# Kernel tuning notes

Hardware: AMD Instinct MI355X
Metric: run time of the kernel (lower is better)

## Reference

```python
import jax, jax.numpy as jnp
import numpy as np

D = 512          # model_dim
H = 4 * D        # hidden_mult * model_dim
E = 8            # n_experts
TEMP = 1.0       # temperature
EPS = 1e-5       # torch LayerNorm eps


def setup_inputs() -> dict:
    key = jax.random.key(0)
    ks = jax.random.split(key, 6)
    x = jax.random.normal(ks[0], (4, 4096, D), dtype=jnp.float32)
    # gate: LayerNorm(D) + Linear(D, E)
    gate_gamma = jnp.ones((D,), jnp.float32)
    gate_beta = jnp.zeros((D,), jnp.float32)
    gate_W = jax.random.normal(ks[1], (D, E), jnp.float32) * 0.02
    gate_b = jnp.zeros((E,), jnp.float32)
    # experts stacked along leading E axis: Linear(D,H) -> LeakyReLU -> Linear(H,D)
    W1 = jax.random.normal(ks[2], (E, D, H), jnp.float32) * 0.02
    b1 = jnp.zeros((E, H), jnp.float32)
    W2 = jax.random.normal(ks[3], (E, H, D), jnp.float32) * 0.02
    b2 = jnp.zeros((E, D), jnp.float32)
    return {"x": x, "gate_gamma": gate_gamma, "gate_beta": gate_beta,
            "gate_W": gate_W, "gate_b": gate_b,
            "W1": W1, "b1": b1, "W2": W2, "b2": b2}


def reference(x, gate_gamma, gate_beta, gate_W, gate_b, W1, b1, W2, b2):
    # gate: LayerNorm then Linear, temperature-scaled softmax
    mu = jnp.mean(x, axis=-1, keepdims=True)
    var = jnp.var(x, axis=-1, keepdims=True)  # biased, as in torch LayerNorm
    xn = (x - mu) * jax.lax.rsqrt(var + EPS) * gate_gamma + gate_beta
    logits = (xn @ gate_W + gate_b) / TEMP          # [B,N,E]
    w = jax.nn.softmax(logits, axis=-1)             # [B,N,E]
    # run every expert on all tokens (faithful to soft routing)
    h = jnp.einsum('bnd,edh->benh', x, W1) + b1[None, :, None, :]  # [B,E,N,H]
    h = jax.nn.leaky_relu(h, negative_slope=0.01)
    y = jnp.einsum('benh,ehd->bend', h, W2) + b2[None, :, None, :]  # [B,E,N,D]
    # gate-weighted combine over experts
    out = jnp.einsum('bend,bne->bnd', y, w)
    return out
```

## Files before the change

### kernel.cpp

```cpp
#include <hip/hip_runtime.h>
#include <stdint.h>

#define TD 512
#define TH 2048
#define TE 8
#define TT 16384

typedef __bf16 bf16x8 __attribute__((ext_vector_type(8)));
typedef __bf16 bf16x4 __attribute__((ext_vector_type(4)));
typedef float  f32x4  __attribute__((ext_vector_type(4)));

__device__ __forceinline__ void async16(const void* src, void* lds) {
    __builtin_amdgcn_global_load_lds((const __attribute__((address_space(1))) uint32_t*)src,
                                     (__attribute__((address_space(3))) uint32_t*)lds,
                                     16, 0, 0);
}

__global__ __launch_bounds__(256) void gate_kernel(
    const float* __restrict__ x, const float* __restrict__ gamma,
    const float* __restrict__ beta, const float* __restrict__ gW,
    const float* __restrict__ gb, const float* __restrict__ b2,
    float* __restrict__ gate_w, __bf16* __restrict__ xb,
    float* __restrict__ outp)
{
    const int t    = blockIdx.x * 4 + (threadIdx.x >> 6);
    const int lane = threadIdx.x & 63;

    const float* xr = x + (size_t)t * TD + lane * 8;
    float4 v0 = *(const float4*)xr;
    float4 v1 = *(const float4*)(xr + 4);
    float xv[8] = {v0.x, v0.y, v0.z, v0.w, v1.x, v1.y, v1.z, v1.w};

    float s = 0.f, sq = 0.f;
    #pragma unroll
    for (int j = 0; j < 8; ++j) { s += xv[j]; sq += xv[j] * xv[j]; }
    #pragma unroll
    for (int off = 32; off > 0; off >>= 1) {
        s  += __shfl_xor(s, off);
        sq += __shfl_xor(sq, off);
    }
    const float mean = s * (1.f / TD);
    const float var  = sq * (1.f / TD) - mean * mean;
    const float rs   = rsqrtf(var + 1e-5f);

    bf16x8 xc;
    #pragma unroll
    for (int j = 0; j < 8; ++j) xc[j] = (__bf16)xv[j];
    *(bf16x8*)&xb[(size_t)t * TD + lane * 8] = xc;

    float p[TE] = {};
    #pragma unroll
    for (int j = 0; j < 8; ++j) {
        const int d = lane * 8 + j;
        const float xn = (xv[j] - mean) * rs * gamma[d] + beta[d];
        const float* wr = gW + (size_t)d * TE;
        #pragma unroll
        for (int e = 0; e < TE; ++e) p[e] += xn * wr[e];
    }
    #pragma unroll
    for (int off = 32; off > 0; off >>= 1) {
        #pragma unroll
        for (int e = 0; e < TE; ++e) p[e] += __shfl_xor(p[e], off);
    }

    float m = -3.4e38f;
    #pragma unroll
    for (int e = 0; e < TE; ++e) { p[e] += gb[e]; m = fmaxf(m, p[e]); }
    float sum = 0.f;
    #pragma unroll
    for (int e = 0; e < TE; ++e) { p[e] = expf(p[e] - m); sum += p[e]; }
    const float inv = 1.f / sum;
    if (lane == 0) {
        #pragma unroll
        for (int e = 0; e < TE; ++e) gate_w[(size_t)t * TE + e] = p[e] * inv;
    }

    float ob[8] = {};
    #pragma unroll
    for (int e = 0; e < TE; ++e) {
        const float we = p[e] * inv;
        const float* b2r = b2 + (size_t)e * TD + lane * 8;
        #pragma unroll
        for (int j = 0; j < 8; ++j) ob[j] += we * b2r[j];
    }
    float4 o0 = {ob[0], ob[1], ob[2], ob[3]};
    float4 o1 = {ob[4], ob[5], ob[6], ob[7]};
    *(float4*)&outp[(size_t)t * TD + lane * 8]     = o0;
    *(float4*)&outp[(size_t)t * TD + lane * 8 + 4] = o1;
}

template <int MODE>
__global__ __launch_bounds__(256) void tcast(
    const float* __restrict__ src, __bf16* __restrict__ dst, int R, int C)
{
    __shared__ __bf16 tile[64][65];
    const int e  = blockIdx.z;
    const int r0 = blockIdx.y * 64, c0 = blockIdx.x * 64;
    const int tr = threadIdx.x >> 6;
    const int tc = threadIdx.x & 63;

    const float* s = src + ((size_t)e * R + r0) * C + c0;
    #pragma unroll
    for (int i = 0; i < 16; ++i) {
        const int r = i * 4 + tr;
        tile[r][tc] = (__bf16)s[(size_t)r * C + tc];
    }
    __syncthreads();

    size_t RS, eoff;
    if (MODE == 0) { RS = (size_t)R;     eoff = (size_t)e * C * R; }
    else           { RS = (size_t)2 * R; eoff = (size_t)(e >> 1) * C * 2 * R + (size_t)(e & 1) * R; }

    __bf16* d = dst + eoff + (size_t)c0 * RS + r0;
    #pragma unroll
    for (int i = 0; i < 16; ++i) {
        const int c = i * 4 + tr;
        d[(size_t)c * RS + tc] = tile[tc][c];
    }
}

template <int EPI>
__global__ __launch_bounds__(256, 2) void gemm2b(
    const __bf16* __restrict__ A, const __bf16* __restrict__ Bt,
    const float* __restrict__ b1, const float* __restrict__ gw,
    void* __restrict__ C, int grp)
{
    constexpr int S  = (EPI == 0) ? TD : 2 * TH;
    constexpr int NT = (EPI == 0) ? 16 : 64;

    __shared__ __align__(16) char smem[49152];

    const int tid  = threadIdx.x;
    const int w    = tid >> 6, lane = tid & 63;
    const int fr   = lane & 15, ks = lane >> 4;

    int bm, bn, e2 = 0, e = 0;
    if (EPI == 0) {
        const int xcd = blockIdx.x & 7, idx = blockIdx.x >> 3;
        bm = xcd * 16 + (idx & 15);
        const int pn = idx >> 4;
        e2 = pn >> 3;
        bn = pn & 7;
        e  = grp * 2 + e2;
        A  += (size_t)bm * 128 * S;
        Bt += (size_t)e2 * TH * TD + (size_t)bn * 256 * S;
        b1 += (size_t)e * TH;
    } else {
        const int xcd = blockIdx.x & 7, idx = blockIdx.x >> 3;
        bm = xcd * 16 + (idx & 15);
        const int pn = idx >> 4;
        const int kh = pn >> 1;
        bn = pn & 1;
        A  += (size_t)bm * 128 * S + (size_t)kh * 2048;
        Bt += (size_t)bn * 256 * S + (size_t)kh * 2048;
    }

    const __bf16* Ab = A;
    const __bf16* Bb = Bt;

    f32x4 acc[8][4] = {};

    auto stage = [&](int t, int b) {
        char* aRegion = smem + b * 8192;
        char* bRegion = smem + 16384 + b * 16384;
        #pragma unroll
        for (int p = 0; p < 2; ++p) {
            const int cid = p * 256 + tid;
            const int row = cid >> 2;
            const int gc  = (cid & 3) ^ ((row >> 1) & 3);
            async16(Ab + (size_t)row * S + t * 32 + gc * 8, aRegion + cid * 16);
        }
        #pragma unroll
        for (int p = 0; p < 4; ++p) {
            const int cid = p * 256 + tid;
            const int row = cid >> 2;
            const int gc  = (cid & 3) ^ ((row >> 1) & 3);
            async16(Bb + (size_t)row * S + t * 32 + gc * 8, bRegion + cid * 16);
        }
    };

    stage(0, 0);
    stage(1, 1);

    for (int t = 0; t < NT; ++t) {
        const int buf = t & 1;
        const char* aR = smem + buf * 8192;
        const char* bR = smem + 16384 + buf * 16384;

        if (t + 1 < NT) { asm volatile("s_waitcnt vmcnt(6)" ::: "memory"); }
        else            { asm volatile("s_waitcnt vmcnt(0)" ::: "memory"); }
        __builtin_amdgcn_sched_barrier(0);
        __builtin_amdgcn_s_barrier();

        bf16x8 areg[8], breg[4];
        #pragma unroll
        for (int m = 0; m < 8; ++m) {
            const int row = m * 16 + fr;
            areg[m] = *(const bf16x8*)(aR + row * 64 + (((ks ^ (row >> 1)) & 3) << 4));
        }
        #pragma unroll
        for (int n = 0; n < 4; ++n) {
            const int row = w * 64 + n * 16 + fr;
            breg[n] = *(const bf16x8*)(bR + row * 64 + (((ks ^ (row >> 1)) & 3) << 4));
        }
        asm volatile("s_waitcnt lgkmcnt(0)" ::: "memory");
        __builtin_amdgcn_sched_barrier(0);
        __builtin_amdgcn_s_barrier();

        if (t + 2 < NT) stage(t + 2, buf);

        __builtin_amdgcn_s_setprio(1);
        #pragma unroll
        for (int m = 0; m < 8; ++m)
            #pragma unroll
            for (int n = 0; n < 4; ++n) {
                if (EPI == 0)
                    acc[m][n] = __builtin_amdgcn_mfma_f32_16x16x32_bf16(breg[n], areg[m], acc[m][n], 0, 0, 0);
                else
                    acc[m][n] = __builtin_amdgcn_mfma_f32_16x16x32_bf16(areg[m], breg[n], acc[m][n], 0, 0, 0);
            }
        __builtin_amdgcn_s_setprio(0);
        __builtin_amdgcn_sched_barrier(0);
    }

    if (EPI == 0) {
        __bf16* hC = (__bf16*)C;
        const int rjc = (lane >> 4) << 2;
        #pragma unroll
        for (int m = 0; m < 8; ++m) {
            const int row = bm * 128 + m * 16 + fr;
            const float wgt = gw[(size_t)row * TE + e];
            __bf16* hrow = hC + (size_t)row * (2 * TH) + e2 * TH;
            #pragma unroll
            for (int n = 0; n < 4; ++n) {
                const int colb = bn * 256 + w * 64 + n * 16 + rjc;
                const f32x4 bv = *(const f32x4*)&b1[colb];
                bf16x4 ov;
                #pragma unroll
                for (int j = 0; j < 4; ++j) {
                    float v = acc[m][n][j] + bv[j];
                    v = v > 0.f ? v : 0.01f * v;
                    ov[j] = (__bf16)(v * wgt);
                }
                *(bf16x4*)&hrow[colb] = ov;
            }
        }
    } else {
        float* oC = (float*)C;
        const int rj = (lane >> 4) << 2;
        #pragma unroll
        for (int m = 0; m < 8; ++m) {
            const int gr0 = bm * 128 + m * 16 + rj;
            #pragma unroll
            for (int j = 0; j < 4; ++j) {
                const int gr = gr0 + j;
                #pragma unroll
                for (int n = 0; n < 4; ++n) {
                    const int gc = bn * 256 + w * 64 + n * 16 + fr;
                    atomicAdd(oC + (size_t)gr * TD + gc, acc[m][n][j]);
                }
            }
        }
    }
}

extern "C" void kernel_launch(void* const* d_in, const int* in_sizes, int n_in,
                              void* d_out, int out_size, void* d_ws, size_t ws_size,
                              hipStream_t stream)
{
    const float* x     = (const float*)d_in[0];
    const float* gamma = (const float*)d_in[1];
    const float* beta  = (const float*)d_in[2];
    const float* gW    = (const float*)d_in[3];
    const float* gb    = (const float*)d_in[4];
    const float* W1    = (const float*)d_in[5];
    const float* b1    = (const float*)d_in[6];
    const float* W2    = (const float*)d_in[7];
    const float* b2    = (const float*)d_in[8];

    char* ws = (char*)d_ws;
    size_t off = 0;
    float*  gate_w = (float*)(ws + off);  off += (size_t)TT * TE * 4;
    __bf16* xb     = (__bf16*)(ws + off); off += (size_t)TT * TD * 2;
    __bf16* W1t    = (__bf16*)(ws + off); off += (size_t)TE * TD * TH * 2;
    __bf16* W2tc   = (__bf16*)(ws + off); off += (size_t)TE * TD * TH * 2;
    __bf16* h      = (__bf16*)(ws + off);

    gate_kernel<<<TT / 4, 256, 0, stream>>>(x, gamma, beta, gW, gb, b2,
                                            gate_w, xb, (float*)d_out);
    tcast<0><<<dim3(TH / 64, TD / 64, TE), 256, 0, stream>>>(W1, W1t, TD, TH);
    tcast<1><<<dim3(TD / 64, TH / 64, TE), 256, 0, stream>>>(W2, W2tc, TH, TD);

    for (int grp = 0; grp < 4; ++grp) {
        gemm2b<0><<<2048, 256, 0, stream>>>(
            xb, W1t + (size_t)grp * 2 * TH * TD, b1, gate_w, (void*)h, grp);
        gemm2b<1><<<512, 256, 0, stream>>>(
            h, W2tc + (size_t)grp * TD * 2 * TH, nullptr, nullptr, d_out, grp);
    }
}
```

Baseline: 847.4 us.

## Load B fragments straight to registers and shrink GEMM tile to 128x128

```diff
diff --git a/kernel.cpp b/kernel.cpp
--- a/kernel.cpp
+++ b/kernel.cpp
@@ -120,7 +120,7 @@
 }
 
 template <int EPI>
-__global__ __launch_bounds__(256, 2) void gemm2b(
+__global__ __launch_bounds__(256, 3) void gemm_rb(
     const __bf16* __restrict__ A, const __bf16* __restrict__ Bt,
     const float* __restrict__ b1, const float* __restrict__ gw,
     void* __restrict__ C, int grp)
@@ -128,112 +128,111 @@
     constexpr int S  = (EPI == 0) ? TD : 2 * TH;
     constexpr int NT = (EPI == 0) ? 16 : 64;
 
-    __shared__ __align__(16) char smem[49152];
+    __shared__ __align__(16) char smem[16384];
 
     const int tid  = threadIdx.x;
     const int w    = tid >> 6, lane = tid & 63;
+    const int wr   = w >> 1, wc = w & 1;
     const int fr   = lane & 15, ks = lane >> 4;
 
     int bm, bn, e2 = 0, e = 0;
     if (EPI == 0) {
-        const int xcd = blockIdx.x & 7, idx = blockIdx.x >> 3;
-        bm = xcd * 16 + (idx & 15);
-        const int pn = idx >> 4;
-        e2 = pn >> 3;
-        bn = pn & 7;
+        bm = blockIdx.x & 127;
+        const int r = blockIdx.x >> 7;
+        bn = r & 15;
+        e2 = r >> 4;
         e  = grp * 2 + e2;
         A  += (size_t)bm * 128 * S;
-        Bt += (size_t)e2 * TH * TD + (size_t)bn * 256 * S;
+        Bt += (size_t)e2 * TH * TD;
         b1 += (size_t)e * TH;
     } else {
-        const int xcd = blockIdx.x & 7, idx = blockIdx.x >> 3;
-        bm = xcd * 16 + (idx & 15);
-        const int pn = idx >> 4;
-        const int kh = pn >> 1;
-        bn = pn & 1;
+        bm = blockIdx.x & 127;
+        const int r = blockIdx.x >> 7;
+        bn = r & 3;
+        const int kh = r >> 2;
         A  += (size_t)bm * 128 * S + (size_t)kh * 2048;
-        Bt += (size_t)bn * 256 * S + (size_t)kh * 2048;
+        Bt += (size_t)kh * 2048;
     }
 
     const __bf16* Ab = A;
-    const __bf16* Bb = Bt;
-
-    f32x4 acc[8][4] = {};
-
-    auto stage = [&](int t, int b) {
-        char* aRegion = smem + b * 8192;
-        char* bRegion = smem + 16384 + b * 16384;
+    const __bf16* Bp = Bt + ((size_t)bn * 128 + wc * 64 + fr) * S + ks * 8;
+
+    f32x4 acc[4][4] = {};
+
+    auto stageA = [&](int t, char* region) {
         #pragma unroll
         for (int p = 0; p < 2; ++p) {
             const int cid = p * 256 + tid;
             const int row = cid >> 2;
             const int gc  = (cid & 3) ^ ((row >> 1) & 3);
-            async16(Ab + (size_t)row * S + t * 32 + gc * 8, aRegion + cid * 16);
-        }
-        #pragma unroll
-        for (int p = 0; p < 4; ++p) {
-            const int cid = p * 256 + tid;
-            const int row = cid >> 2;
-            const int gc  = (cid & 3) ^ ((row >> 1) & 3);
-            async16(Bb + (size_t)row * S + t * 32 + gc * 8, bRegion + cid * 16);
+            async16(Ab + (size_t)row * S + t * 32 + gc * 8, region + cid * 16);
         }
     };
-
-    stage(0, 0);
-    stage(1, 1);
-
-    for (int t = 0; t < NT; ++t) {
-        const int buf = t & 1;
-        const char* aR = smem + buf * 8192;
-        const char* bR = smem + 16384 + buf * 16384;
-
-        if (t + 1 < NT) { asm volatile("s_waitcnt vmcnt(6)" ::: "memory"); }
+    auto loadB = [&](int t, bf16x8 (&dst)[4]) {
+        #pragma unroll
+        for (int n = 0; n < 4; ++n)
+            dst[n] = *(const bf16x8*)(Bp + (size_t)n * 16 * S + t * 32);
+    };
+
+    auto iter = [&](int t, char* buf, bf16x8 (&cur)[4], bf16x8 (&nxt)[4]) {
+        if (t + 1 < NT) { asm volatile("s_waitcnt vmcnt(2)" ::: "memory"); }
         else            { asm volatile("s_waitcnt vmcnt(0)" ::: "memory"); }
         __builtin_amdgcn_sched_barrier(0);
         __builtin_amdgcn_s_barrier();
 
-        bf16x8 areg[8], breg[4];
-        #pragma unroll
-        for (int m = 0; m < 8; ++m) {
-            const int row = m * 16 + fr;
-            areg[m] = *(const bf16x8*)(aR + row * 64 + (((ks ^ (row >> 1)) & 3) << 4));
-        }
-        #pragma unroll
-        for (int n = 0; n < 4; ++n) {
-            const int row = w * 64 + n * 16 + fr;
-            breg[n] = *(const bf16x8*)(bR + row * 64 + (((ks ^ (row >> 1)) & 3) << 4));
+        bf16x8 areg[4];
+        #pragma unroll
+        for (int m = 0; m < 4; ++m) {
+            const int row = wr * 64 + m * 16 + fr;
+            areg[m] = *(const bf16x8*)(buf + row * 64 + (((ks ^ (row >> 1)) & 3) << 4));
         }
         asm volatile("s_waitcnt lgkmcnt(0)" ::: "memory");
         __builtin_amdgcn_sched_barrier(0);
         __builtin_amdgcn_s_barrier();
 
-        if (t + 2 < NT) stage(t + 2, buf);
+        if (t + 1 < NT) loadB(t + 1, nxt);
+        __builtin_amdgcn_sched_barrier(0);
+        if (t + 2 < NT) stageA(t + 2, buf);
+        __builtin_amdgcn_sched_barrier(0);
 
         __builtin_amdgcn_s_setprio(1);
         #pragma unroll
-        for (int m = 0; m < 8; ++m)
+        for (int m = 0; m < 4; ++m)
             #pragma unroll
             for (int n = 0; n < 4; ++n) {
                 if (EPI == 0)
-                    acc[m][n] = __builtin_amdgcn_mfma_f32_16x16x32_bf16(breg[n], areg[m], acc[m][n], 0, 0, 0);
+                    acc[m][n] = __builtin_amdgcn_mfma_f32_16x16x32_bf16(cur[n], areg[m], acc[m][n], 0, 0, 0);
                 else
-                    acc[m][n] = __builtin_amdgcn_mfma_f32_16x16x32_bf16(areg[m], breg[n], acc[m][n], 0, 0, 0);
+                    acc[m][n] = __builtin_amdgcn_mfma_f32_16x16x32_bf16(areg[m], cur[n], acc[m][n], 0, 0, 0);
             }
         __builtin_amdgcn_s_setprio(0);
         __builtin_amdgcn_sched_barrier(0);
+    };
+
+    bf16x8 bregA[4], bregB[4];
+    char* buf0 = smem;
+    char* buf1 = smem + 8192;
+
+    loadB(0, bregA);
+    stageA(0, buf0);
+    stageA(1, buf1);
+
+    for (int tt = 0; tt < NT; tt += 2) {
+        iter(tt,     buf0, bregA, bregB);
+        iter(tt + 1, buf1, bregB, bregA);
     }
 
     if (EPI == 0) {
         __bf16* hC = (__bf16*)C;
         const int rjc = (lane >> 4) << 2;
         #pragma unroll
-        for (int m = 0; m < 8; ++m) {
-            const int row = bm * 128 + m * 16 + fr;
+        for (int m = 0; m < 4; ++m) {
+            const int row = bm * 128 + wr * 64 + m * 16 + fr;
             const float wgt = gw[(size_t)row * TE + e];
             __bf16* hrow = hC + (size_t)row * (2 * TH) + e2 * TH;
             #pragma unroll
             for (int n = 0; n < 4; ++n) {
-                const int colb = bn * 256 + w * 64 + n * 16 + rjc;
+                const int colb = bn * 128 + wc * 64 + n * 16 + rjc;
                 const f32x4 bv = *(const f32x4*)&b1[colb];
                 bf16x4 ov;
                 #pragma unroll
@@ -249,14 +248,14 @@
         float* oC = (float*)C;
         const int rj = (lane >> 4) << 2;
         #pragma unroll
-        for (int m = 0; m < 8; ++m) {
-            const int gr0 = bm * 128 + m * 16 + rj;
+        for (int m = 0; m < 4; ++m) {
+            const int gr0 = bm * 128 + wr * 64 + m * 16 + rj;
             #pragma unroll
             for (int j = 0; j < 4; ++j) {
                 const int gr = gr0 + j;
                 #pragma unroll
                 for (int n = 0; n < 4; ++n) {
-                    const int gc = bn * 256 + w * 64 + n * 16 + fr;
+                    const int gc = bn * 128 + wc * 64 + n * 16 + fr;
                     atomicAdd(oC + (size_t)gr * TD + gc, acc[m][n][j]);
                 }
             }
@@ -292,9 +291,9 @@
     tcast<1><<<dim3(TD / 64, TH / 64, TE), 256, 0, stream>>>(W2, W2tc, TH, TD);
 
     for (int grp = 0; grp < 4; ++grp) {
-        gemm2b<0><<<2048, 256, 0, stream>>>(
+        gemm_rb<0><<<4096, 256, 0, stream>>>(
             xb, W1t + (size_t)grp * 2 * TH * TD, b1, gate_w, (void*)h, grp);
-        gemm2b<1><<<512, 256, 0, stream>>>(
+        gemm_rb<1><<<1024, 256, 0, stream>>>(
             h, W2tc + (size_t)grp * TD * 2 * TH, nullptr, nullptr, d_out, grp);
     }
 }
```

Result: slower. 1.432 ms (+69.0%).

## Keep A tile resident in LDS for first GEMM and stream all B panels

Applied to the files above, without the earlier changes.

```diff
diff --git a/kernel.cpp b/kernel.cpp
--- a/kernel.cpp
+++ b/kernel.cpp
@@ -119,14 +119,124 @@
     }
 }
 
-template <int EPI>
-__global__ __launch_bounds__(256, 2) void gemm2b(
+__global__ __launch_bounds__(512, 2) void gemm1res(
     const __bf16* __restrict__ A, const __bf16* __restrict__ Bt,
     const float* __restrict__ b1, const float* __restrict__ gw,
-    void* __restrict__ C, int grp)
-{
-    constexpr int S  = (EPI == 0) ? TD : 2 * TH;
-    constexpr int NT = (EPI == 0) ? 16 : 64;
+    __bf16* __restrict__ hC, int grp)
+{
+    __shared__ __align__(16) char smem[163840];
+    char* Asm = smem;
+    char* Bsm = smem + 131072;
+
+    const int tid  = threadIdx.x;
+    const int w    = tid >> 6, lane = tid & 63;
+    const int wr   = w >> 2, wc = w & 3;
+    const int fr   = lane & 15, ks = lane >> 4;
+
+    const int bm = blockIdx.x & 127;
+    const int e2 = blockIdx.x >> 7;
+    const int e  = grp * 2 + e2;
+
+    const __bf16* Ab  = A  + (size_t)bm * 128 * TD;
+    const __bf16* Bb  = Bt + (size_t)e2 * TH * TD;
+    const float*  b1e = b1 + (size_t)e * TH;
+
+    #pragma unroll
+    for (int q = 0; q < 16; ++q) {
+        const int cid = q * 512 + tid;
+        const int row = cid >> 6;
+        const int c   = cid & 63;
+        async16(Ab + (size_t)row * TD + (size_t)(c ^ (row & 7)) * 8,
+                Asm + cid * 16);
+    }
+
+    auto stageB = [&](int bt, char* region) {
+        const int p = bt >> 4, kt = bt & 15;
+        const __bf16* Bp = Bb + (size_t)p * 256 * TD + kt * 32;
+        #pragma unroll
+        for (int q = 0; q < 2; ++q) {
+            const int cid = q * 512 + tid;
+            const int row = cid >> 2;
+            const int c   = cid & 3;
+            async16(Bp + (size_t)row * TD + (size_t)(c ^ ((row >> 1) & 3)) * 8,
+                    region + cid * 16);
+        }
+    };
+
+    stageB(0, Bsm);
+    stageB(1, Bsm + 16384);
+
+    f32x4 acc[4][4] = {};
+    constexpr int BT = 128;
+
+    for (int bt = 0; bt < BT; ++bt) {
+        const int kt = bt & 15;
+        char* buf = Bsm + (bt & 1) * 16384;
+
+        if (bt + 1 < BT) { asm volatile("s_waitcnt vmcnt(2)" ::: "memory"); }
+        else             { asm volatile("s_waitcnt vmcnt(0)" ::: "memory"); }
+        __builtin_amdgcn_sched_barrier(0);
+        __builtin_amdgcn_s_barrier();
+        __builtin_amdgcn_sched_barrier(0);
+
+        bf16x8 areg[4], breg[4];
+        #pragma unroll
+        for (int m = 0; m < 4; ++m) {
+            const int row = wr * 64 + m * 16 + fr;
+            const int c   = kt * 4 + ks;
+            areg[m] = *(const bf16x8*)(Asm + row * 1024 + (size_t)((c ^ (row & 7)) << 4));
+        }
+        #pragma unroll
+        for (int n = 0; n < 4; ++n) {
+            const int row = wc * 64 + n * 16 + fr;
+            breg[n] = *(const bf16x8*)(buf + row * 64 + (((ks ^ (row >> 1)) & 3) << 4));
+        }
+        __builtin_amdgcn_s_setprio(1);
+        #pragma unroll
+        for (int m = 0; m < 4; ++m)
+            #pragma unroll
+            for (int n = 0; n < 4; ++n)
+                acc[m][n] = __builtin_amdgcn_mfma_f32_16x16x32_bf16(breg[n], areg[m], acc[m][n], 0, 0, 0);
+        __builtin_amdgcn_s_setprio(0);
+        __builtin_amdgcn_sched_barrier(0);
+        __builtin_amdgcn_s_barrier();
+        __builtin_amdgcn_sched_barrier(0);
+
+        if (bt + 2 < BT) stageB(bt + 2, buf);
+
+        if (kt == 15) {
+            const int p   = bt >> 4;
+            const int rjc = (lane >> 4) << 2;
+            #pragma unroll
+            for (int m = 0; m < 4; ++m) {
+                const int row = bm * 128 + wr * 64 + m * 16 + fr;
+                const float wgt = gw[(size_t)row * TE + e];
+                __bf16* hrow = hC + (size_t)row * (2 * TH) + e2 * TH;
+                #pragma unroll
+                for (int n = 0; n < 4; ++n) {
+                    const int colb = p * 256 + wc * 64 + n * 16 + rjc;
+                    const f32x4 bv = *(const f32x4*)&b1e[colb];
+                    bf16x4 ov;
+                    #pragma unroll
+                    for (int j = 0; j < 4; ++j) {
+                        float v = acc[m][n][j] + bv[j];
+                        v = v > 0.f ? v : 0.01f * v;
+                        ov[j] = (__bf16)(v * wgt);
+                        acc[m][n][j] = 0.f;
+                    }
+                    *(bf16x4*)&hrow[colb] = ov;
+                }
+            }
+        }
+    }
+}
+
+__global__ __launch_bounds__(256, 2) void gemm2(
+    const __bf16* __restrict__ A, const __bf16* __restrict__ Bt,
+    float* __restrict__ oC)
+{
+    constexpr int S  = 2 * TH;
+    constexpr int NT = 64;
 
     __shared__ __align__(16) char smem[49152];
 
@@ -134,29 +244,14 @@
     const int w    = tid >> 6, lane = tid & 63;
     const int fr   = lane & 15, ks = lane >> 4;
 
-    int bm, bn, e2 = 0, e = 0;
-    if (EPI == 0) {
-        const int xcd = blockIdx.x & 7, idx = blockIdx.x >> 3;
-        bm = xcd * 16 + (idx & 15);
-        const int pn = idx >> 4;
-        e2 = pn >> 3;
-        bn = pn & 7;
-        e  = grp * 2 + e2;
-        A  += (size_t)bm * 128 * S;
-        Bt += (size_t)e2 * TH * TD + (size_t)bn * 256 * S;
-        b1 += (size_t)e * TH;
-    } else {
-        const int xcd = blockIdx.x & 7, idx = blockIdx.x >> 3;
-        bm = xcd * 16 + (idx & 15);
-        const int pn = idx >> 4;
-        const int kh = pn >> 1;
-        bn = pn & 1;
-        A  += (size_t)bm * 128 * S + (size_t)kh * 2048;
-        Bt += (size_t)bn * 256 * S + (size_t)kh * 2048;
-    }
-
-    const __bf16* Ab = A;
-    const __bf16* Bb = Bt;
+    const int xcd = blockIdx.x & 7, idx = blockIdx.x >> 3;
+    const int bm  = xcd * 16 + (idx & 15);
+    const int pn  = idx >> 4;
+    const int kh  = pn >> 1;
+    const int bn  = pn & 1;
+
+    const __bf16* Ab = A  + (size_t)bm * 128 * S + (size_t)kh * 2048;
+    const __bf16* Bb = Bt + (size_t)bn * 256 * S + (size_t)kh * 2048;
 
     f32x4 acc[8][4] = {};
 
@@ -191,6 +286,7 @@
         else            { asm volatile("s_waitcnt vmcnt(0)" ::: "memory"); }
         __builtin_amdgcn_sched_barrier(0);
         __builtin_amdgcn_s_barrier();
+        __builtin_amdgcn_sched_barrier(0);
 
         bf16x8 areg[8], breg[4];
         #pragma unroll
@@ -203,62 +299,31 @@
             const int row = w * 64 + n * 16 + fr;
             breg[n] = *(const bf16x8*)(bR + row * 64 + (((ks ^ (row >> 1)) & 3) << 4));
         }
-        asm volatile("s_waitcnt lgkmcnt(0)" ::: "memory");
-        __builtin_amdgcn_sched_barrier(0);
-        __builtin_amdgcn_s_barrier();
-
-        if (t + 2 < NT) stage(t + 2, buf);
-
         __builtin_amdgcn_s_setprio(1);
         #pragma unroll
         for (int m = 0; m < 8; ++m)
             #pragma unroll
-            for (int n = 0; n < 4; ++n) {
-                if (EPI == 0)
-                    acc[m][n] = __builtin_amdgcn_mfma_f32_16x16x32_bf16(breg[n], areg[m], acc[m][n], 0, 0, 0);
-                else
-                    acc[m][n] = __builtin_amdgcn_mfma_f32_16x16x32_bf16(areg[m], breg[n], acc[m][n], 0, 0, 0);
-            }
+            for (int n = 0; n < 4; ++n)
+                acc[m][n] = __builtin_amdgcn_mfma_f32_16x16x32_bf16(areg[m], breg[n], acc[m][n], 0, 0, 0);
         __builtin_amdgcn_s_setprio(0);
         __builtin_amdgcn_sched_barrier(0);
-    }
-
-    if (EPI == 0) {
-        __bf16* hC = (__bf16*)C;
-        const int rjc = (lane >> 4) << 2;
-        #pragma unroll
-        for (int m = 0; m < 8; ++m) {
-            const int row = bm * 128 + m * 16 + fr;
-            const float wgt = gw[(size_t)row * TE + e];
-            __bf16* hrow = hC + (size_t)row * (2 * TH) + e2 * TH;
+        __builtin_amdgcn_s_barrier();
+        __builtin_amdgcn_sched_barrier(0);
+
+        if (t + 2 < NT) stage(t + 2, buf);
+    }
+
+    const int rj = (lane >> 4) << 2;
+    #pragma unroll
+    for (int m = 0; m < 8; ++m) {
+        const int gr0 = bm * 128 + m * 16 + rj;
+        #pragma unroll
+        for (int j = 0; j < 4; ++j) {
+            const int gr = gr0 + j;
             #pragma unroll
             for (int n = 0; n < 4; ++n) {
-                const int colb = bn * 256 + w * 64 + n * 16 + rjc;
-                const f32x4 bv = *(const f32x4*)&b1[colb];
-                bf16x4 ov;
-                #pragma unroll
-                for (int j = 0; j < 4; ++j) {
-                    float v = acc[m][n][j] + bv[j];
-                    v = v > 0.f ? v : 0.01f * v;
-                    ov[j] = (__bf16)(v * wgt);
-                }
-                *(bf16x4*)&hrow[colb] = ov;
-            }
-        }
-    } else {
-        float* oC = (float*)C;
-        const int rj = (lane >> 4) << 2;
-        #pragma unroll
-        for (int m = 0; m < 8; ++m) {
-            const int gr0 = bm * 128 + m * 16 + rj;
-            #pragma unroll
-            for (int j = 0; j < 4; ++j) {
-                const int gr = gr0 + j;
-                #pragma unroll
-                for (int n = 0; n < 4; ++n) {
-                    const int gc = bn * 256 + w * 64 + n * 16 + fr;
-                    atomicAdd(oC + (size_t)gr * TD + gc, acc[m][n][j]);
-                }
+                const int gc = bn * 256 + w * 64 + n * 16 + fr;
+                atomicAdd(oC + (size_t)gr * TD + gc, acc[m][n][j]);
             }
         }
     }
@@ -292,9 +357,9 @@
     tcast<1><<<dim3(TD / 64, TH / 64, TE), 256, 0, stream>>>(W2, W2tc, TH, TD);
 
     for (int grp = 0; grp < 4; ++grp) {
-        gemm2b<0><<<2048, 256, 0, stream>>>(
-            xb, W1t + (size_t)grp * 2 * TH * TD, b1, gate_w, (void*)h, grp);
-        gemm2b<1><<<512, 256, 0, stream>>>(
-            h, W2tc + (size_t)grp * TD * 2 * TH, nullptr, nullptr, d_out, grp);
-    }
-}
+        gemm1res<<<256, 512, 0, stream>>>(
+            xb, W1t + (size_t)grp * 2 * TH * TD, b1, gate_w, h, grp);
+        gemm2<<<512, 256, 0, stream>>>(
+            h, W2tc + (size_t)grp * TD * 2 * TH, (float*)d_out);
+    }
+}
```

Result: slower. 909.9 us (+7.4%).
